# Kernel optimization log

Measured on AMD Instinct MI355X. Metric: run time of the kernel, lower is better.

The kernel has to match this reference:

```python
import jax, jax.numpy as jnp
import numpy as np

EPS = 1e-8  # torch F.cosine_similarity eps


def setup_inputs() -> dict:
    key = jax.random.key(0)
    B, CAP, CD, CTX = 32, 32768, 64, 64
    ks = jax.random.split(key, 9)
    inp = {
        "query_content": jax.random.normal(ks[0], (B, CD), jnp.float32),
        "query_context": jax.random.normal(ks[1], (B, CTX), jnp.float32),
        "memory_content": 0.1 * jax.random.normal(ks[2], (CAP, CD), jnp.float32),
        "memory_contexts": 0.1 * jax.random.normal(ks[3], (CAP, CTX), jnp.float32),
        "memory_freshness": jnp.ones((CAP,), jnp.float32),
        "W1": jax.random.normal(ks[4], (2 * CD, CD), jnp.float32) / np.sqrt(2 * CD),
        "b1": 0.01 * jax.random.normal(ks[5], (CD,), jnp.float32),
        "W2": jax.random.normal(ks[6], (CD, 1), jnp.float32) / np.sqrt(CD),
        "b2": 0.01 * jax.random.normal(ks[7], (1,), jnp.float32),
        "top_k": 16,
    }
    return inp


def reference(query_content, query_context, memory_content, memory_contexts,
              memory_freshness, W1, b1, W2, b2, top_k):
    B, CD = query_content.shape
    # similarity_calculator MLP over all (query, memory) pairs.
    # Linear on concat([q, m]) == q @ W1[:CD] + m @ W1[CD:]  (avoids the concat).
    q_part = query_content @ W1[:CD]            # [B, CD]
    m_part = memory_content @ W1[CD:]           # [CAP, CD]
    h = jax.nn.relu(q_part[:, None, :] + m_part[None, :, :] + b1)  # [B, CAP, CD]
    content_sim = jax.nn.sigmoid(jnp.einsum('bch,h->bc', h, W2[:, 0]) + b2[0])  # [B, CAP]

    # cosine similarity between query_context and each stored context
    qn = query_context / jnp.maximum(jnp.linalg.norm(query_context, axis=-1, keepdims=True), EPS)
    mn = memory_contexts / jnp.maximum(jnp.linalg.norm(memory_contexts, axis=-1, keepdims=True), EPS)
    context_sim = qn @ mn.T                      # [B, CAP]

    time_weights = memory_freshness              # time_mask is all-ones in source
    final = 0.5 * content_sim + 0.3 * context_sim + 0.2 * time_weights[None, :]

    top_similarities, top_indices = jax.lax.top_k(final, top_k)   # [B, k]
    retrieved_content = memory_content[top_indices]               # [B, k, CD]
    retrieved_time_weights = time_weights[top_indices]            # [B, k]
    return (retrieved_content, top_similarities, retrieved_time_weights)
```

## Files before the change

kernel.cpp:

```cpp
#include <hip/hip_runtime.h>
#include <math.h>

#define CAP   32768
#define NB    32
#define CD    64
#define ROWS  64
#define NBLK  (CAP / ROWS)
#define TOPK  16
#define CEPS  1e-8f

#define WS_QP    0
#define WS_QN    2048
#define WS_FINAL 4096

#define PITCH 68

#define CHUNK 2048
#define NCHUNK (CAP / CHUNK)

__global__ __launch_bounds__(64) void prep_kernel(
    const float* __restrict__ qc,
    const float* __restrict__ qctx,
    const float* __restrict__ W1,
    const float* __restrict__ b1,
    float* __restrict__ ws)
{
    const int b = blockIdx.x;
    const int j = threadIdx.x;

    float a0 = b1[j], a1 = 0.f, a2 = 0.f, a3 = 0.f;
    #pragma unroll
    for (int i = 0; i < 64; i += 4) {
        a0 = fmaf(qc[b * 64 + i + 0], W1[(i + 0) * 64 + j], a0);
        a1 = fmaf(qc[b * 64 + i + 1], W1[(i + 1) * 64 + j], a1);
        a2 = fmaf(qc[b * 64 + i + 2], W1[(i + 2) * 64 + j], a2);
        a3 = fmaf(qc[b * 64 + i + 3], W1[(i + 3) * 64 + j], a3);
    }
    ws[WS_QP + b * 64 + j] = (a0 + a1) + (a2 + a3);

    float x = qctx[b * 64 + j];
    float ss = x * x;
    ss += __shfl_xor(ss, 1,  64);
    ss += __shfl_xor(ss, 2,  64);
    ss += __shfl_xor(ss, 4,  64);
    ss += __shfl_xor(ss, 8,  64);
    ss += __shfl_xor(ss, 16, 64);
    ss += __shfl_xor(ss, 32, 64);
    float nrm = fmaxf(sqrtf(ss), CEPS);
    ws[WS_QN + b * 64 + j] = x / nrm;
}

__device__ __forceinline__ void acc_pair(const float4 qp, const float4 qn,
                                         const float4 m, const float4 xv,
                                         const float4 w2, float& a1, float& a2)
{
    a1 = fmaf(fmaxf(qp.x + m.x, 0.f), w2.x, a1);
    a1 = fmaf(fmaxf(qp.y + m.y, 0.f), w2.y, a1);
    a1 = fmaf(fmaxf(qp.z + m.z, 0.f), w2.z, a1);
    a1 = fmaf(fmaxf(qp.w + m.w, 0.f), w2.w, a1);
    a2 = fmaf(qn.x, xv.x, a2);
    a2 = fmaf(qn.y, xv.y, a2);
    a2 = fmaf(qn.z, xv.z, a2);
    a2 = fmaf(qn.w, xv.w, a2);
}

__global__ __launch_bounds__(256) void score_kernel(
    const float* __restrict__ mcont,
    const float* __restrict__ mctx,
    const float* __restrict__ fresh,
    const float* __restrict__ W1,
    const float* __restrict__ W2,
    const float* __restrict__ b2,
    float* __restrict__ ws)
{
    __shared__ float s_mc[ROWS * PITCH];
    __shared__ float s_mx[ROWS * PITCH];
    __shared__ float s_mp[ROWS * PITCH];
    __shared__ float s_qp[NB * PITCH];
    __shared__ float s_qn[NB * PITCH];
    __shared__ float s_w2[64];
    __shared__ float s_base[ROWS];
    __shared__ float s_inv[ROWS];

    const int tid = threadIdx.x;
    const int lane = tid & 63;
    const int C0 = blockIdx.x * ROWS;

    const float4* g_mc = (const float4*)(mcont + (size_t)C0 * 64);
    const float4* g_mx = (const float4*)(mctx  + (size_t)C0 * 64);
    #pragma unroll
    for (int t = tid; t < ROWS * 16; t += 256) {
        int r = t >> 4, c4 = t & 15;
        *(float4*)&s_mc[r * PITCH + c4 * 4] = g_mc[t];
        *(float4*)&s_mx[r * PITCH + c4 * 4] = g_mx[t];
    }
    const float4* g_qp = (const float4*)(ws + WS_QP);
    const float4* g_qn = (const float4*)(ws + WS_QN);
    #pragma unroll
    for (int t = tid; t < NB * 16; t += 256) {
        int r = t >> 4, c4 = t & 15;
        *(float4*)&s_qp[r * PITCH + c4 * 4] = g_qp[t];
        *(float4*)&s_qn[r * PITCH + c4 * 4] = g_qn[t];
    }
    if (tid < 64) {
        s_w2[tid]   = W2[tid];
        s_base[tid] = 0.2f * fresh[C0 + tid];
    }

    float w1c[64];
    #pragma unroll
    for (int i = 0; i < 64; ++i)
        w1c[i] = W1[(64 + i) * 64 + lane];

    __syncthreads();

    const int wv = tid >> 6;
    for (int r = 0; r < 16; ++r) {
        const int c = wv * 16 + r;
        const float* row = &s_mc[c * PITCH];
        float a0 = 0.f, a1 = 0.f, a2 = 0.f, a3 = 0.f;
        #pragma unroll
        for (int i4 = 0; i4 < 16; i4 += 4) {
            float4 m0 = *(const float4*)&row[(i4 + 0) * 4];
            float4 m1 = *(const float4*)&row[(i4 + 1) * 4];
            float4 m2 = *(const float4*)&row[(i4 + 2) * 4];
            float4 m3 = *(const float4*)&row[(i4 + 3) * 4];
            a0 = fmaf(m0.x, w1c[4*i4+ 0], a0); a0 = fmaf(m0.y, w1c[4*i4+ 1], a0);
            a0 = fmaf(m0.z, w1c[4*i4+ 2], a0); a0 = fmaf(m0.w, w1c[4*i4+ 3], a0);
            a1 = fmaf(m1.x, w1c[4*i4+ 4], a1); a1 = fmaf(m1.y, w1c[4*i4+ 5], a1);
            a1 = fmaf(m1.z, w1c[4*i4+ 6], a1); a1 = fmaf(m1.w, w1c[4*i4+ 7], a1);
            a2 = fmaf(m2.x, w1c[4*i4+ 8], a2); a2 = fmaf(m2.y, w1c[4*i4+ 9], a2);
            a2 = fmaf(m2.z, w1c[4*i4+10], a2); a2 = fmaf(m2.w, w1c[4*i4+11], a2);
            a3 = fmaf(m3.x, w1c[4*i4+12], a3); a3 = fmaf(m3.y, w1c[4*i4+13], a3);
            a3 = fmaf(m3.z, w1c[4*i4+14], a3); a3 = fmaf(m3.w, w1c[4*i4+15], a3);
        }
        s_mp[c * PITCH + lane] = (a0 + a1) + (a2 + a3);

        float x = s_mx[c * PITCH + lane];
        float ss = x * x;
        ss += __shfl_xor(ss, 1,  64);
        ss += __shfl_xor(ss, 2,  64);
        ss += __shfl_xor(ss, 4,  64);
        ss += __shfl_xor(ss, 8,  64);
        ss += __shfl_xor(ss, 16, 64);
        ss += __shfl_xor(ss, 32, 64);
        if (lane == 0)
            s_inv[c] = 0.3f / fmaxf(sqrtf(ss), CEPS);
    }
    __syncthreads();

    const int bq = (tid & 15) << 1;
    const int cq = (tid >> 4) << 2;
    float a1[2][4] = {{0.f}}, a2[2][4] = {{0.f}};

    #pragma unroll 4
    for (int j4 = 0; j4 < 16; ++j4) {
        const int jo = j4 * 4;
        float4 w2v  = *(const float4*)&s_w2[jo];
        float4 qp0  = *(const float4*)&s_qp[ bq      * PITCH + jo];
        float4 qp1  = *(const float4*)&s_qp[(bq + 1) * PITCH + jo];
        float4 qn0  = *(const float4*)&s_qn[ bq      * PITCH + jo];
        float4 qn1  = *(const float4*)&s_qn[(bq + 1) * PITCH + jo];
        #pragma unroll
        for (int ci = 0; ci < 4; ++ci) {
            float4 mv = *(const float4*)&s_mp[(cq + ci) * PITCH + jo];
            float4 xv = *(const float4*)&s_mx[(cq + ci) * PITCH + jo];
            acc_pair(qp0, qn0, mv, xv, w2v, a1[0][ci], a2[0][ci]);
            acc_pair(qp1, qn1, mv, xv, w2v, a1[1][ci], a2[1][ci]);
        }
    }

    const float b2v = b2[0];
    #pragma unroll
    for (int bi = 0; bi < 2; ++bi) {
        #pragma unroll
        for (int ci = 0; ci < 4; ++ci) {
            const int b = bq + bi, c = cq + ci;
            float logit = a1[bi][ci] + b2v;
            float sig = 0.5f / (1.f + expf(-logit));
            s_mc[b * PITCH + c] = sig + a2[bi][ci] * s_inv[c] + s_base[c];
        }
    }
    __syncthreads();

    #pragma unroll
    for (int it = 0; it < 2; ++it) {
        int idx = it * 256 + tid;
        int b = idx >> 4, c4 = idx & 15;
        *(float4*)&ws[WS_FINAL + (size_t)b * CAP + C0 + c4 * 4] =
            *(const float4*)&s_mc[b * PITCH + c4 * 4];
    }
}

__global__ __launch_bounds__(64) void topk_part1(float* __restrict__ ws)
{
    const int lane = threadIdx.x;
    const int b = blockIdx.y;
    float* row = ws + WS_FINAL + (size_t)b * CAP;
    const int cbase = blockIdx.x * CHUNK;

    float v[32];
    #pragma unroll
    for (int j = 0; j < 32; ++j)
        v[j] = row[cbase + j * 64 + lane];

    float outv = 0.f;
    int   outi = 0;

    for (int k = 0; k < TOPK; ++k) {
        float bv = v[0]; int bj = 0;
        #pragma unroll
        for (int j = 1; j < 32; ++j)
            if (v[j] > bv) { bv = v[j]; bj = j; }
        int bi = cbase + bj * 64 + lane;

        #pragma unroll
        for (int off = 1; off < 64; off <<= 1) {
            float ov = __shfl_xor(bv, off, 64);
            int   oi = __shfl_xor(bi, off, 64);
            if (ov > bv || (ov == bv && oi < bi)) { bv = ov; bi = oi; }
        }
        if (lane == k) { outv = bv; outi = bi; }

        int rel = bi - cbase;
        bool mine = ((rel & 63) == lane);
        int wj = rel >> 6;
        #pragma unroll
        for (int j = 0; j < 32; ++j)
            if (mine && wj == j) v[j] = -INFINITY;
    }

    if (lane < TOPK) {
        row[cbase + lane]        = outv;
        row[cbase + TOPK + lane] = __int_as_float(outi);
    }
}

__global__ __launch_bounds__(64) void topk_part2(
    const float* __restrict__ mcont,
    const float* __restrict__ fresh,
    const float* __restrict__ ws,
    float* __restrict__ out)
{
    const int lane = threadIdx.x;
    const int b = blockIdx.x;
    const float* row = ws + WS_FINAL + (size_t)b * CAP;

    float* out_content = out;
    float* out_sim     = out + NB * TOPK * 64;
    float* out_tw      = out + NB * TOPK * 64 + NB * TOPK;

    const int chunk = lane & 15;
    const int s0 = lane >> 4;
    float v[4]; int iv[4];
    #pragma unroll
    for (int s = 0; s < 4; ++s) {
        v[s]  = row[chunk * CHUNK + s0 + 4 * s];
        iv[s] = __float_as_int(row[chunk * CHUNK + TOPK + s0 + 4 * s]);
    }

    float wval = 0.f; int widx = 0;
    for (int k = 0; k < TOPK; ++k) {
        float bv = v[0]; int bi = iv[0];
        #pragma unroll
        for (int s = 1; s < 4; ++s)
            if (v[s] > bv || (v[s] == bv && iv[s] < bi)) { bv = v[s]; bi = iv[s]; }
        #pragma unroll
        for (int off = 1; off < 64; off <<= 1) {
            float ov = __shfl_xor(bv, off, 64);
            int   oi = __shfl_xor(bi, off, 64);
            if (ov > bv || (ov == bv && oi < bi)) { bv = ov; bi = oi; }
        }
        if (lane == k) { wval = bv; widx = bi; }
        #pragma unroll
        for (int s = 0; s < 4; ++s)
            if (iv[s] == bi) v[s] = -INFINITY;
    }

    if (lane < TOPK) {
        out_sim[b * TOPK + lane] = wval;
        out_tw [b * TOPK + lane] = fresh[widx];
    }

    #pragma unroll
    for (int r = 0; r < TOPK; ++r) {
        int wi = __shfl(widx, r, 64);
        out_content[(size_t)b * TOPK * 64 + r * 64 + lane] =
            mcont[(size_t)wi * 64 + lane];
    }
}

extern "C" void kernel_launch(void* const* d_in, const int* in_sizes, int n_in,
                              void* d_out, int out_size, void* d_ws, size_t ws_size,
                              hipStream_t stream) {
    const float* qc    = (const float*)d_in[0];
    const float* qctx  = (const float*)d_in[1];
    const float* mcont = (const float*)d_in[2];
    const float* mctx  = (const float*)d_in[3];
    const float* fresh = (const float*)d_in[4];
    const float* W1    = (const float*)d_in[5];
    const float* b1    = (const float*)d_in[6];
    const float* W2    = (const float*)d_in[7];
    const float* b2    = (const float*)d_in[8];
    float* out = (float*)d_out;
    float* ws  = (float*)d_ws;

    prep_kernel<<<NB, 64, 0, stream>>>(qc, qctx, W1, b1, ws);
    score_kernel<<<NBLK, 256, 0, stream>>>(mcont, mctx, fresh, W1, W2, b2, ws);
    topk_part1<<<dim3(NCHUNK, NB), 64, 0, stream>>>(ws);
    topk_part2<<<NB, 64, 0, stream>>>(mcont, fresh, ws, out);
}
```

Measured before the change: 144.4 us.

## Fuse query prep into score kernel and restructure memory projection

```diff
diff --git a/kernel.cpp b/kernel.cpp
--- a/kernel.cpp
+++ b/kernel.cpp
@@ -3,184 +3,175 @@
 
 #define CAP   32768
 #define NB    32
-#define CD    64
 #define ROWS  64
 #define NBLK  (CAP / ROWS)
 #define TOPK  16
 #define CEPS  1e-8f
 
-#define WS_QP    0
-#define WS_QN    2048
-#define WS_FINAL 4096
-
 #define PITCH 68
-
 #define CHUNK 2048
 #define NCHUNK (CAP / CHUNK)
 
-__global__ __launch_bounds__(64) void prep_kernel(
+#define WS_FINAL 0
+
+__global__ __launch_bounds__(256) void score_kernel(
     const float* __restrict__ qc,
     const float* __restrict__ qctx,
-    const float* __restrict__ W1,
-    const float* __restrict__ b1,
-    float* __restrict__ ws)
-{
-    const int b = blockIdx.x;
-    const int j = threadIdx.x;
-
-    float a0 = b1[j], a1 = 0.f, a2 = 0.f, a3 = 0.f;
-    #pragma unroll
-    for (int i = 0; i < 64; i += 4) {
-        a0 = fmaf(qc[b * 64 + i + 0], W1[(i + 0) * 64 + j], a0);
-        a1 = fmaf(qc[b * 64 + i + 1], W1[(i + 1) * 64 + j], a1);
-        a2 = fmaf(qc[b * 64 + i + 2], W1[(i + 2) * 64 + j], a2);
-        a3 = fmaf(qc[b * 64 + i + 3], W1[(i + 3) * 64 + j], a3);
-    }
-    ws[WS_QP + b * 64 + j] = (a0 + a1) + (a2 + a3);
-
-    float x = qctx[b * 64 + j];
-    float ss = x * x;
-    ss += __shfl_xor(ss, 1,  64);
-    ss += __shfl_xor(ss, 2,  64);
-    ss += __shfl_xor(ss, 4,  64);
-    ss += __shfl_xor(ss, 8,  64);
-    ss += __shfl_xor(ss, 16, 64);
-    ss += __shfl_xor(ss, 32, 64);
-    float nrm = fmaxf(sqrtf(ss), CEPS);
-    ws[WS_QN + b * 64 + j] = x / nrm;
-}
-
-__device__ __forceinline__ void acc_pair(const float4 qp, const float4 qn,
-                                         const float4 m, const float4 xv,
-                                         const float4 w2, float& a1, float& a2)
-{
-    a1 = fmaf(fmaxf(qp.x + m.x, 0.f), w2.x, a1);
-    a1 = fmaf(fmaxf(qp.y + m.y, 0.f), w2.y, a1);
-    a1 = fmaf(fmaxf(qp.z + m.z, 0.f), w2.z, a1);
-    a1 = fmaf(fmaxf(qp.w + m.w, 0.f), w2.w, a1);
-    a2 = fmaf(qn.x, xv.x, a2);
-    a2 = fmaf(qn.y, xv.y, a2);
-    a2 = fmaf(qn.z, xv.z, a2);
-    a2 = fmaf(qn.w, xv.w, a2);
-}
-
-__global__ __launch_bounds__(256) void score_kernel(
     const float* __restrict__ mcont,
     const float* __restrict__ mctx,
     const float* __restrict__ fresh,
     const float* __restrict__ W1,
+    const float* __restrict__ b1,
     const float* __restrict__ W2,
     const float* __restrict__ b2,
     float* __restrict__ ws)
 {
-    __shared__ float s_mc[ROWS * PITCH];
-    __shared__ float s_mx[ROWS * PITCH];
     __shared__ float s_mp[ROWS * PITCH];
     __shared__ float s_qp[NB * PITCH];
     __shared__ float s_qn[NB * PITCH];
-    __shared__ float s_w2[64];
+    __shared__ float s_out[NB * PITCH];
     __shared__ float s_base[ROWS];
     __shared__ float s_inv[ROWS];
 
     const int tid = threadIdx.x;
-    const int lane = tid & 63;
     const int C0 = blockIdx.x * ROWS;
 
-    const float4* g_mc = (const float4*)(mcont + (size_t)C0 * 64);
-    const float4* g_mx = (const float4*)(mctx  + (size_t)C0 * 64);
-    #pragma unroll
-    for (int t = tid; t < ROWS * 16; t += 256) {
-        int r = t >> 4, c4 = t & 15;
-        *(float4*)&s_mc[r * PITCH + c4 * 4] = g_mc[t];
-        *(float4*)&s_mx[r * PITCH + c4 * 4] = g_mx[t];
-    }
-    const float4* g_qp = (const float4*)(ws + WS_QP);
-    const float4* g_qn = (const float4*)(ws + WS_QN);
-    #pragma unroll
-    for (int t = tid; t < NB * 16; t += 256) {
-        int r = t >> 4, c4 = t & 15;
-        *(float4*)&s_qp[r * PITCH + c4 * 4] = g_qp[t];
-        *(float4*)&s_qn[r * PITCH + c4 * 4] = g_qn[t];
+    {
+        const int b = tid >> 3, sl = tid & 7, j0 = sl * 8;
+        const float* qrow = qc + b * 64;
+        float acc[8];
+        #pragma unroll
+        for (int jj = 0; jj < 8; ++jj) acc[jj] = b1[j0 + jj];
+        #pragma unroll 4
+        for (int i = 0; i < 64; ++i) {
+            float q = qrow[i];
+            float4 wa = *(const float4*)&W1[i * 64 + j0];
+            float4 wb = *(const float4*)&W1[i * 64 + j0 + 4];
+            acc[0] = fmaf(q, wa.x, acc[0]); acc[1] = fmaf(q, wa.y, acc[1]);
+            acc[2] = fmaf(q, wa.z, acc[2]); acc[3] = fmaf(q, wa.w, acc[3]);
+            acc[4] = fmaf(q, wb.x, acc[4]); acc[5] = fmaf(q, wb.y, acc[5]);
+            acc[6] = fmaf(q, wb.z, acc[6]); acc[7] = fmaf(q, wb.w, acc[7]);
+        }
+        #pragma unroll
+        for (int jj = 0; jj < 8; ++jj) s_qp[b * PITCH + j0 + jj] = acc[jj];
+
+        const float* xrow = qctx + b * 64;
+        float ss = 0.f;
+        #pragma unroll
+        for (int i4 = 0; i4 < 16; ++i4) {
+            float4 x = *(const float4*)&xrow[i4 * 4];
+            ss = fmaf(x.x, x.x, ss); ss = fmaf(x.y, x.y, ss);
+            ss = fmaf(x.z, x.z, ss); ss = fmaf(x.w, x.w, ss);
+        }
+        float rinv = 1.f / fmaxf(sqrtf(ss), CEPS);
+        #pragma unroll
+        for (int g = 0; g < 2; ++g) {
+            float4 x = *(const float4*)&xrow[j0 + g * 4];
+            s_qn[b * PITCH + j0 + g * 4 + 0] = x.x * rinv;
+            s_qn[b * PITCH + j0 + g * 4 + 1] = x.y * rinv;
+            s_qn[b * PITCH + j0 + g * 4 + 2] = x.z * rinv;
+            s_qn[b * PITCH + j0 + g * 4 + 3] = x.w * rinv;
+        }
     }
     if (tid < 64) {
-        s_w2[tid]   = W2[tid];
+        const float* xr = mctx + (size_t)(C0 + tid) * 64;
+        float ss = 0.f;
+        #pragma unroll
+        for (int i4 = 0; i4 < 16; ++i4) {
+            float4 x = *(const float4*)&xr[i4 * 4];
+            ss = fmaf(x.x, x.x, ss); ss = fmaf(x.y, x.y, ss);
+            ss = fmaf(x.z, x.z, ss); ss = fmaf(x.w, x.w, ss);
+        }
+        s_inv[tid]  = 0.3f / fmaxf(sqrtf(ss), CEPS);
         s_base[tid] = 0.2f * fresh[C0 + tid];
     }
-
-    float w1c[64];
-    #pragma unroll
-    for (int i = 0; i < 64; ++i)
-        w1c[i] = W1[(64 + i) * 64 + lane];
-
     __syncthreads();
 
-    const int wv = tid >> 6;
-    for (int r = 0; r < 16; ++r) {
-        const int c = wv * 16 + r;
-        const float* row = &s_mc[c * PITCH];
-        float a0 = 0.f, a1 = 0.f, a2 = 0.f, a3 = 0.f;
-        #pragma unroll
-        for (int i4 = 0; i4 < 16; i4 += 4) {
-            float4 m0 = *(const float4*)&row[(i4 + 0) * 4];
-            float4 m1 = *(const float4*)&row[(i4 + 1) * 4];
-            float4 m2 = *(const float4*)&row[(i4 + 2) * 4];
-            float4 m3 = *(const float4*)&row[(i4 + 3) * 4];
-            a0 = fmaf(m0.x, w1c[4*i4+ 0], a0); a0 = fmaf(m0.y, w1c[4*i4+ 1], a0);
-            a0 = fmaf(m0.z, w1c[4*i4+ 2], a0); a0 = fmaf(m0.w, w1c[4*i4+ 3], a0);
-            a1 = fmaf(m1.x, w1c[4*i4+ 4], a1); a1 = fmaf(m1.y, w1c[4*i4+ 5], a1);
-            a1 = fmaf(m1.z, w1c[4*i4+ 6], a1); a1 = fmaf(m1.w, w1c[4*i4+ 7], a1);
-            a2 = fmaf(m2.x, w1c[4*i4+ 8], a2); a2 = fmaf(m2.y, w1c[4*i4+ 9], a2);
-            a2 = fmaf(m2.z, w1c[4*i4+10], a2); a2 = fmaf(m2.w, w1c[4*i4+11], a2);
-            a3 = fmaf(m3.x, w1c[4*i4+12], a3); a3 = fmaf(m3.y, w1c[4*i4+13], a3);
-            a3 = fmaf(m3.z, w1c[4*i4+14], a3); a3 = fmaf(m3.w, w1c[4*i4+15], a3);
-        }
-        s_mp[c * PITCH + lane] = (a0 + a1) + (a2 + a3);
-
-        float x = s_mx[c * PITCH + lane];
-        float ss = x * x;
-        ss += __shfl_xor(ss, 1,  64);
-        ss += __shfl_xor(ss, 2,  64);
-        ss += __shfl_xor(ss, 4,  64);
-        ss += __shfl_xor(ss, 8,  64);
-        ss += __shfl_xor(ss, 16, 64);
-        ss += __shfl_xor(ss, 32, 64);
-        if (lane == 0)
-            s_inv[c] = 0.3f / fmaxf(sqrtf(ss), CEPS);
+    {
+        const int c_lo = tid & 15;
+        const int j0 = (tid >> 4) * 4;
+        float acc[4][4] = {{0.f}};
+        const float* mrow = mcont + (size_t)(C0 + c_lo) * 64;
+        #pragma unroll 4
+        for (int i4 = 0; i4 < 16; ++i4) {
+            float4 w0 = *(const float4*)&W1[(64 + i4 * 4 + 0) * 64 + j0];
+            float4 w1r = *(const float4*)&W1[(64 + i4 * 4 + 1) * 64 + j0];
+            float4 w2r = *(const float4*)&W1[(64 + i4 * 4 + 2) * 64 + j0];
+            float4 w3r = *(const float4*)&W1[(64 + i4 * 4 + 3) * 64 + j0];
+            #pragma unroll
+            for (int ci = 0; ci < 4; ++ci) {
+                float4 m = *(const float4*)&mrow[ci * 1024 + i4 * 4];
+                acc[ci][0] = fmaf(m.x, w0.x, acc[ci][0]);
+                acc[ci][1] = fmaf(m.x, w0.y, acc[ci][1]);
+                acc[ci][2] = fmaf(m.x, w0.z, acc[ci][2]);
+                acc[ci][3] = fmaf(m.x, w0.w, acc[ci][3]);
+                acc[ci][0] = fmaf(m.y, w1r.x, acc[ci][0]);
+                acc[ci][1] = fmaf(m.y, w1r.y, acc[ci][1]);
+                acc[ci][2] = fmaf(m.y, w1r.z, acc[ci][2]);
+                acc[ci][3] = fmaf(m.y, w1r.w, acc[ci][3]);
+                acc[ci][0] = fmaf(m.z, w2r.x, acc[ci][0]);
+                acc[ci][1] = fmaf(m.z, w2r.y, acc[ci][1]);
+                acc[ci][2] = fmaf(m.z, w2r.z, acc[ci][2]);
+                acc[ci][3] = fmaf(m.z, w2r.w, acc[ci][3]);
+                acc[ci][0] = fmaf(m.w, w3r.x, acc[ci][0]);
+                acc[ci][1] = fmaf(m.w, w3r.y, acc[ci][1]);
+                acc[ci][2] = fmaf(m.w, w3r.z, acc[ci][2]);
+                acc[ci][3] = fmaf(m.w, w3r.w, acc[ci][3]);
+            }
+        }
+        #pragma unroll
+        for (int ci = 0; ci < 4; ++ci)
+            *(float4*)&s_mp[(c_lo + 16 * ci) * PITCH + j0] =
+                make_float4(acc[ci][0], acc[ci][1], acc[ci][2], acc[ci][3]);
     }
     __syncthreads();
 
     const int bq = (tid & 15) << 1;
     const int cq = (tid >> 4) << 2;
     float a1[2][4] = {{0.f}}, a2[2][4] = {{0.f}};
+    const float* mxb = mctx + (size_t)C0 * 64;
 
     #pragma unroll 4
     for (int j4 = 0; j4 < 16; ++j4) {
         const int jo = j4 * 4;
-        float4 w2v  = *(const float4*)&s_w2[jo];
-        float4 qp0  = *(const float4*)&s_qp[ bq      * PITCH + jo];
-        float4 qp1  = *(const float4*)&s_qp[(bq + 1) * PITCH + jo];
-        float4 qn0  = *(const float4*)&s_qn[ bq      * PITCH + jo];
-        float4 qn1  = *(const float4*)&s_qn[(bq + 1) * PITCH + jo];
+        float4 w2v = *(const float4*)(W2 + jo);
+        float4 qp0 = *(const float4*)&s_qp[ bq      * PITCH + jo];
+        float4 qp1 = *(const float4*)&s_qp[(bq + 1) * PITCH + jo];
+        float4 qn0 = *(const float4*)&s_qn[ bq      * PITCH + jo];
+        float4 qn1 = *(const float4*)&s_qn[(bq + 1) * PITCH + jo];
         #pragma unroll
         for (int ci = 0; ci < 4; ++ci) {
             float4 mv = *(const float4*)&s_mp[(cq + ci) * PITCH + jo];
-            float4 xv = *(const float4*)&s_mx[(cq + ci) * PITCH + jo];
-            acc_pair(qp0, qn0, mv, xv, w2v, a1[0][ci], a2[0][ci]);
-            acc_pair(qp1, qn1, mv, xv, w2v, a1[1][ci], a2[1][ci]);
+            float4 xv = *(const float4*)&mxb[(cq + ci) * 64 + jo];
+            a1[0][ci] = fmaf(fmaxf(qp0.x + mv.x, 0.f), w2v.x, a1[0][ci]);
+            a1[0][ci] = fmaf(fmaxf(qp0.y + mv.y, 0.f), w2v.y, a1[0][ci]);
+            a1[0][ci] = fmaf(fmaxf(qp0.z + mv.z, 0.f), w2v.z, a1[0][ci]);
+            a1[0][ci] = fmaf(fmaxf(qp0.w + mv.w, 0.f), w2v.w, a1[0][ci]);
+            a2[0][ci] = fmaf(qn0.x, xv.x, a2[0][ci]);
+            a2[0][ci] = fmaf(qn0.y, xv.y, a2[0][ci]);
+            a2[0][ci] = fmaf(qn0.z, xv.z, a2[0][ci]);
+            a2[0][ci] = fmaf(qn0.w, xv.w, a2[0][ci]);
+            a1[1][ci] = fmaf(fmaxf(qp1.x + mv.x, 0.f), w2v.x, a1[1][ci]);
+            a1[1][ci] = fmaf(fmaxf(qp1.y + mv.y, 0.f), w2v.y, a1[1][ci]);
+            a1[1][ci] = fmaf(fmaxf(qp1.z + mv.z, 0.f), w2v.z, a1[1][ci]);
+            a1[1][ci] = fmaf(fmaxf(qp1.w + mv.w, 0.f), w2v.w, a1[1][ci]);
+            a2[1][ci] = fmaf(qn1.x, xv.x, a2[1][ci]);
+            a2[1][ci] = fmaf(qn1.y, xv.y, a2[1][ci]);
+            a2[1][ci] = fmaf(qn1.z, xv.z, a2[1][ci]);
+            a2[1][ci] = fmaf(qn1.w, xv.w, a2[1][ci]);
         }
     }
 
     const float b2v = b2[0];
     #pragma unroll
-    for (int bi = 0; bi < 2; ++bi) {
+    for (int bi = 0; bi < 2; ++bi)
         #pragma unroll
         for (int ci = 0; ci < 4; ++ci) {
             const int b = bq + bi, c = cq + ci;
             float logit = a1[bi][ci] + b2v;
             float sig = 0.5f / (1.f + expf(-logit));
-            s_mc[b * PITCH + c] = sig + a2[bi][ci] * s_inv[c] + s_base[c];
-        }
-    }
+            s_out[b * PITCH + c] = sig + a2[bi][ci] * s_inv[c] + s_base[c];
+        }
     __syncthreads();
 
     #pragma unroll
@@ -188,7 +179,7 @@
         int idx = it * 256 + tid;
         int b = idx >> 4, c4 = idx & 15;
         *(float4*)&ws[WS_FINAL + (size_t)b * CAP + C0 + c4 * 4] =
-            *(const float4*)&s_mc[b * PITCH + c4 * 4];
+            *(const float4*)&s_out[b * PITCH + c4 * 4];
     }
 }
 
@@ -201,8 +192,11 @@
 
     float v[32];
     #pragma unroll
-    for (int j = 0; j < 32; ++j)
-        v[j] = row[cbase + j * 64 + lane];
+    for (int g = 0; g < 8; ++g) {
+        float4 t = *(const float4*)&row[cbase + g * 256 + lane * 4];
+        v[4 * g + 0] = t.x; v[4 * g + 1] = t.y;
+        v[4 * g + 2] = t.z; v[4 * g + 3] = t.w;
+    }
 
     float outv = 0.f;
     int   outi = 0;
@@ -212,7 +206,7 @@
         #pragma unroll
         for (int j = 1; j < 32; ++j)
             if (v[j] > bv) { bv = v[j]; bj = j; }
-        int bi = cbase + bj * 64 + lane;
+        int bi = cbase + (bj >> 2) * 256 + lane * 4 + (bj & 3);
 
         #pragma unroll
         for (int off = 1; off < 64; off <<= 1) {
@@ -223,8 +217,8 @@
         if (lane == k) { outv = bv; outi = bi; }
 
         int rel = bi - cbase;
-        bool mine = ((rel & 63) == lane);
-        int wj = rel >> 6;
+        bool mine = (((rel >> 2) & 63) == lane);
+        int wj = ((rel >> 8) << 2) | (rel & 3);
         #pragma unroll
         for (int j = 0; j < 32; ++j)
             if (mine && wj == j) v[j] = -INFINITY;
@@ -305,8 +299,8 @@
     float* out = (float*)d_out;
     float* ws  = (float*)d_ws;
 
-    prep_kernel<<<NB, 64, 0, stream>>>(qc, qctx, W1, b1, ws);
-    score_kernel<<<NBLK, 256, 0, stream>>>(mcont, mctx, fresh, W1, W2, b2, ws);
+    score_kernel<<<NBLK, 256, 0, stream>>>(qc, qctx, mcont, mctx, fresh,
+                                           W1, b1, W2, b2, ws);
     topk_part1<<<dim3(NCHUNK, NB), 64, 0, stream>>>(ws);
     topk_part2<<<NB, 64, 0, stream>>>(mcont, fresh, ws, out);
 }
```

After: 153.4 us. +6.2%, slower.
